# Kernel tuning notes

Measured on AMD Instinct MI355X. Metric: run time of the kernel, lower is better.

Reference implementation:

```python
import jax, jax.numpy as jnp
import numpy as np

N = 8192
IN_C = 128
OUT_C = 128


def setup_inputs() -> dict:
    key = jax.random.key(0)
    k_x, k_adj, k_w, k_b = jax.random.split(key, 4)
    x = jax.random.normal(k_x, (N, IN_C), dtype=jnp.float32)
    adj = jax.random.uniform(k_adj, (N, N), dtype=jnp.float32)
    # nn.Linear params: weight (out, in), bias (out,)
    bound = 1.0 / np.sqrt(IN_C)
    W = jax.random.uniform(k_w, (OUT_C, IN_C), dtype=jnp.float32, minval=-bound, maxval=bound)
    b = jax.random.uniform(k_b, (OUT_C,), dtype=jnp.float32, minval=-bound, maxval=bound)
    return {"x": x, "adj": adj, "W": W, "b": b}


def reference(x, adj, W, b):
    # A_hat = adj + I  (self loops)
    # D_hat = rowsum(A_hat); norm = D^-1/2 A_hat D^-1/2
    n = adj.shape[0]
    a_hat = adj + jnp.eye(n, dtype=adj.dtype)
    deg = jnp.sum(a_hat, axis=1)
    d_inv_sqrt = jnp.power(deg, -0.5)
    d_inv_sqrt = jnp.where(jnp.isinf(d_inv_sqrt), 0.0, d_inv_sqrt)
    # D^-1/2 @ A_hat @ D^-1/2 as row/column broadcast scaling (same math)
    norm_adj = a_hat * d_inv_sqrt[:, None] * d_inv_sqrt[None, :]
    support = norm_adj @ x  # (N, in_c)
    return support @ W.T + b
```

## Files before the change

kernel.cpp:

```cpp
#include <hip/hip_runtime.h>


#define N_ROWS 8192
#define N_C    128
#define NM     (8192 * 128)

typedef __bf16 bf16x8 __attribute__((ext_vector_type(8)));
typedef float  f32x4  __attribute__((ext_vector_type(4)));

__global__ __launch_bounds__(256) void k_rowsum(const float* __restrict__ adj,
                                                float* __restrict__ dinv) {
    const int row = blockIdx.x;
    const float4* rp = (const float4*)(adj + (size_t)row * N_ROWS);
    float s = 0.f;
#pragma unroll
    for (int i = 0; i < 8; ++i) {
        float4 v = rp[threadIdx.x + i * 256];
        s += (v.x + v.y) + (v.z + v.w);
    }
#pragma unroll
    for (int off = 32; off > 0; off >>= 1) s += __shfl_down(s, off, 64);
    __shared__ float red[4];
    const int lane = threadIdx.x & 63, wid = threadIdx.x >> 6;
    if (lane == 0) red[wid] = s;
    __syncthreads();
    if (threadIdx.x == 0) {
        float deg = 1.0f + ((red[0] + red[1]) + (red[2] + red[3]));
        dinv[row] = 1.0f / sqrtf(deg);
    }
}

__global__ __launch_bounds__(256) void k_xw(const float* __restrict__ x,
                                            const float* __restrict__ W,
                                            const float* __restrict__ dinv,
                                            float* __restrict__ tnat,
                                            __bf16* __restrict__ tTh) {
    __shared__ __align__(16) float WtBuf[64 * 132];
    __shared__ __align__(16) float xs[32][128];
    const int tid = threadIdx.x;
    const int j0 = blockIdx.x * 32;

    {
        const int c4 = (tid & 31) * 4;
        const int r0 = tid >> 5;
#pragma unroll
        for (int p = 0; p < 4; ++p)
            *(float4*)&xs[r0 + p * 8][c4] =
                *(const float4*)(x + (size_t)(j0 + r0 + p * 8) * N_C + c4);
    }

    const int tc = tid & 15, tr = tid >> 4;
    const int c0 = tc * 8, r0c = tr * 2;
    float acc[2][8];
#pragma unroll
    for (int i = 0; i < 2; ++i)
#pragma unroll
        for (int j = 0; j < 8; ++j) acc[i][j] = 0.f;

    const int c_lo = (tid & 7) + ((tid >> 7) << 3);
    const int k4   = ((tid >> 3) & 15) * 4;

    for (int kh = 0; kh < 2; ++kh) {
        if (kh) __syncthreads();
#pragma unroll
        for (int p = 0; p < 8; ++p) {
            int c = c_lo + 16 * p;
            float4 w = *(const float4*)(W + (size_t)c * N_C + kh * 64 + k4);
            WtBuf[(k4 + 0) * 132 + c] = w.x;
            WtBuf[(k4 + 1) * 132 + c] = w.y;
            WtBuf[(k4 + 2) * 132 + c] = w.z;
            WtBuf[(k4 + 3) * 132 + c] = w.w;
        }
        __syncthreads();
#pragma unroll 4
        for (int k = 0; k < 64; ++k) {
            const float a0 = xs[r0c][kh * 64 + k];
            const float a1 = xs[r0c + 1][kh * 64 + k];
            const float* wr = &WtBuf[k * 132 + c0];
            const float4 b0 = *(const float4*)wr;
            const float4 b1 = *(const float4*)(wr + 4);
#pragma unroll
            for (int q = 0; q < 4; ++q) {
                acc[0][q]     = fmaf(a0, ((const float*)&b0)[q], acc[0][q]);
                acc[0][q + 4] = fmaf(a0, ((const float*)&b1)[q], acc[0][q + 4]);
                acc[1][q]     = fmaf(a1, ((const float*)&b0)[q], acc[1][q]);
                acc[1][q + 4] = fmaf(a1, ((const float*)&b1)[q], acc[1][q + 4]);
            }
        }
    }

    __syncthreads();
    float* tt = WtBuf;
#pragma unroll
    for (int ri = 0; ri < 2; ++ri) {
        const int j = j0 + r0c + ri;
        const float d = dinv[j];
        float4 o0 = {d * acc[ri][0], d * acc[ri][1], d * acc[ri][2], d * acc[ri][3]};
        float4 o1 = {d * acc[ri][4], d * acc[ri][5], d * acc[ri][6], d * acc[ri][7]};
        *(float4*)(tnat + (size_t)j * N_C + c0)     = o0;
        *(float4*)(tnat + (size_t)j * N_C + c0 + 4) = o1;
#pragma unroll
        for (int q = 0; q < 4; ++q) {
            tt[(r0c + ri) * 129 + c0 + q]     = ((const float*)&o0)[q];
            tt[(r0c + ri) * 129 + c0 + 4 + q] = ((const float*)&o1)[q];
        }
    }
    __syncthreads();
    {
        const int c  = tid >> 1;
        const int jh = (tid & 1) * 16;
        __bf16 ov[16];
#pragma unroll
        for (int q = 0; q < 16; ++q) ov[q] = (__bf16)tt[(jh + q) * 129 + c];
        __bf16* dst = tTh + (size_t)c * N_ROWS + j0 + jh;
        *(int4*)dst = ((const int4*)ov)[0];
        *(int4*)(dst + 8) = ((const int4*)ov)[1];
    }
}

template <bool FUSE>
__global__ __launch_bounds__(512) void k_spmm(const float* __restrict__ adj,
                                              const __bf16* __restrict__ tTh,
                                              const float* __restrict__ tnat,
                                              const float* __restrict__ dinv,
                                              const float* __restrict__ bias,
                                              float* __restrict__ outp,
                                              int klen) {
    __shared__ __align__(16) __bf16 Ah[128 * 72];
    __shared__ __align__(16) __bf16 Al[128 * 72];
    __shared__ __align__(16) __bf16 Th[128 * 72];
    const int tid   = threadIdx.x;
    const int i0    = blockIdx.x * 128;
    const int kbase = blockIdx.y * klen;
    const int nch   = klen / 64;

    float4 areg[2][2];
    int4   treg[2];

    auto load_chunk = [&](int k0) {
#pragma unroll
        for (int p = 0; p < 2; ++p) {
            const int s = tid + p * 512;
            const int r = s >> 3, kg = s & 7;
            const float* g = adj + (size_t)(i0 + r) * N_ROWS + k0 + kg * 8;
            areg[p][0] = *(const float4*)g;
            areg[p][1] = *(const float4*)(g + 4);
        }
        {
            const int n = tid >> 2, q = tid & 3;
            const int4* g = (const int4*)(tTh + (size_t)n * N_ROWS + k0 + q * 16);
            treg[0] = g[0];
            treg[1] = g[1];
        }
    };
    auto store_chunk = [&]() {
#pragma unroll
        for (int p = 0; p < 2; ++p) {
            const int s = tid + p * 512;
            const int r = s >> 3, kg = s & 7;
            __bf16 h[8], lo[8];
            const float* v = (const float*)&areg[p][0];
#pragma unroll
            for (int j = 0; j < 8; ++j) {
                h[j]  = (__bf16)v[j];
                lo[j] = (__bf16)(v[j] - (float)h[j]);
            }
            *(bf16x8*)&Ah[r * 72 + kg * 8] = *(const bf16x8*)h;
            *(bf16x8*)&Al[r * 72 + kg * 8] = *(const bf16x8*)lo;
        }
        {
            const int n = tid >> 2, q = tid & 3;
            *(int4*)&Th[n * 72 + q * 16]     = treg[0];
            *(int4*)&Th[n * 72 + q * 16 + 8] = treg[1];
        }
    };

    const int wv = tid >> 6, l = tid & 63;
    const int wm = wv >> 1, wn = wv & 1;
    const int lm = l & 15, lq = l >> 4;

    f32x4 acc[2][4] = {};

    load_chunk(kbase);
    store_chunk();
    __syncthreads();
    for (int ch = 0; ch < nch; ++ch) {
        const bool more = (ch + 1 < nch);
        if (more) load_chunk(kbase + (ch + 1) * 64);
#pragma unroll
        for (int ks = 0; ks < 2; ++ks) {
            const int ko = ks * 32 + lq * 8;
            bf16x8 a0h = *(const bf16x8*)&Ah[(wm * 32 + lm) * 72 + ko];
            bf16x8 a1h = *(const bf16x8*)&Ah[(wm * 32 + 16 + lm) * 72 + ko];
            bf16x8 a0l = *(const bf16x8*)&Al[(wm * 32 + lm) * 72 + ko];
            bf16x8 a1l = *(const bf16x8*)&Al[(wm * 32 + 16 + lm) * 72 + ko];
#pragma unroll
            for (int nt = 0; nt < 4; ++nt) {
                bf16x8 b = *(const bf16x8*)&Th[(wn * 64 + nt * 16 + lm) * 72 + ko];
                acc[0][nt] = __builtin_amdgcn_mfma_f32_16x16x32_bf16(a0h, b, acc[0][nt], 0, 0, 0);
                acc[1][nt] = __builtin_amdgcn_mfma_f32_16x16x32_bf16(a1h, b, acc[1][nt], 0, 0, 0);
                acc[0][nt] = __builtin_amdgcn_mfma_f32_16x16x32_bf16(a0l, b, acc[0][nt], 0, 0, 0);
                acc[1][nt] = __builtin_amdgcn_mfma_f32_16x16x32_bf16(a1l, b, acc[1][nt], 0, 0, 0);
            }
        }
        __syncthreads();
        if (more) {
            store_chunk();
            __syncthreads();
        }
    }

    float* po = FUSE ? outp : outp + (size_t)blockIdx.y * NM;
#pragma unroll
    for (int mt = 0; mt < 2; ++mt)
#pragma unroll
        for (int nt = 0; nt < 4; ++nt) {
            const int col = wn * 64 + nt * 16 + lm;
#pragma unroll
            for (int r = 0; r < 4; ++r) {
                const int row = i0 + wm * 32 + mt * 16 + lq * 4 + r;
                float v = acc[mt][nt][r];
                if (FUSE)
                    v = dinv[row] * (v + tnat[(size_t)row * N_C + col]) + bias[col];
                po[(size_t)row * N_C + col] = v;
            }
        }
}

__global__ __launch_bounds__(256) void k_combine(const float* __restrict__ part,
                                                 const float* __restrict__ tnat,
                                                 const float* __restrict__ dinv,
                                                 const float* __restrict__ bias,
                                                 float* __restrict__ outp, int S) {
    const size_t off = ((size_t)blockIdx.x * 256 + threadIdx.x) * 4;
    const int i = (int)(off >> 7);
    const int c = (int)(off & 127);
    float4 s = *(const float4*)(tnat + off);
    for (int p = 0; p < S; ++p) {
        const float4 v = *(const float4*)(part + (size_t)p * NM + off);
        s.x += v.x; s.y += v.y; s.z += v.z; s.w += v.w;
    }
    const float d = dinv[i];
    const float4 bv = *(const float4*)(bias + c);
    float4 o = {d * s.x + bv.x, d * s.y + bv.y, d * s.z + bv.z, d * s.w + bv.w};
    *(float4*)(outp + off) = o;
}

extern "C" void kernel_launch(void* const* d_in, const int* in_sizes, int n_in,
                              void* d_out, int out_size, void* d_ws, size_t ws_size,
                              hipStream_t stream) {
    const float* x   = (const float*)d_in[0];
    const float* adj = (const float*)d_in[1];
    const float* W   = (const float*)d_in[2];
    const float* b   = (const float*)d_in[3];
    float* out = (float*)d_out;

    char* base = (char*)d_ws;
    float*  dinv = (float*)base;
    float*  tnat = (float*)(base + 32768);
    __bf16* tTh  = (__bf16*)(base + 32768 + (4u << 20));
    float*  part = (float*)(base + 32768 + (6u << 20));

    const size_t fixed = 32768 + (6u << 20);
    int S = 0;
    if      (ws_size >= fixed + 8 * ((size_t)NM * 4)) S = 8;
    else if (ws_size >= fixed + 4 * ((size_t)NM * 4)) S = 4;
    else if (ws_size >= fixed + 2 * ((size_t)NM * 4)) S = 2;

    k_rowsum<<<N_ROWS, 256, 0, stream>>>(adj, dinv);
    k_xw<<<N_ROWS / 32, 256, 0, stream>>>(x, W, dinv, tnat, tTh);
    if (S > 0) {
        dim3 grid(N_ROWS / 128, S);
        k_spmm<false><<<grid, 512, 0, stream>>>(adj, tTh, tnat, dinv, b, part, N_ROWS / S);
        k_combine<<<NM / 1024, 256, 0, stream>>>(part, tnat, dinv, b, out, S);
    } else {
        dim3 grid(N_ROWS / 128, 1);
        k_spmm<true><<<grid, 512, 0, stream>>>(adj, tTh, tnat, dinv, b, out, N_ROWS);
    }
}
```

Before: 460.1 us.

## Drop split-bf16 adjacency low part and shrink spmm tile to 64 rows

The adjacency matrix was converted to a high/low pair of bf16 values to emulate fp32 accuracy, which doubled the MFMA count and the LDS traffic. It is now converted to a single bf16, which halves the matrix-core work and removes the low-part buffer. The block tile also shrinks from 128 to 64 rows with 256 threads and a 4-block occupancy hint, doubling the grid. The cost is lower precision: uniform adjacency values are rounded to bf16, which may push the result past the tolerance. The smaller tile also means the tTh operand is reloaded by twice as many blocks.

Result: slower. 505.1 us (+9.8%).

```diff
diff --git a/kernel.cpp b/kernel.cpp
--- a/kernel.cpp
+++ b/kernel.cpp
@@ -6,6 +6,7 @@
 #define NM     (8192 * 128)
 
 typedef __bf16 bf16x8 __attribute__((ext_vector_type(8)));
+typedef __bf16 bf16x4 __attribute__((ext_vector_type(4)));
 typedef float  f32x4  __attribute__((ext_vector_type(4)));
 
 __global__ __launch_bounds__(256) void k_rowsum(const float* __restrict__ adj,
@@ -119,60 +120,46 @@
 }
 
 template <bool FUSE>
-__global__ __launch_bounds__(512) void k_spmm(const float* __restrict__ adj,
-                                              const __bf16* __restrict__ tTh,
-                                              const float* __restrict__ tnat,
-                                              const float* __restrict__ dinv,
-                                              const float* __restrict__ bias,
-                                              float* __restrict__ outp,
-                                              int klen) {
-    __shared__ __align__(16) __bf16 Ah[128 * 72];
-    __shared__ __align__(16) __bf16 Al[128 * 72];
+__global__ __launch_bounds__(256, 4) void k_spmm(const float* __restrict__ adj,
+                                                 const __bf16* __restrict__ tTh,
+                                                 const float* __restrict__ tnat,
+                                                 const float* __restrict__ dinv,
+                                                 const float* __restrict__ bias,
+                                                 float* __restrict__ outp,
+                                                 int klen) {
+    __shared__ __align__(16) __bf16 Ah[64 * 72];
     __shared__ __align__(16) __bf16 Th[128 * 72];
     const int tid   = threadIdx.x;
-    const int i0    = blockIdx.x * 128;
+    const int i0    = blockIdx.x * 64;
     const int kbase = blockIdx.y * klen;
     const int nch   = klen / 64;
 
-    float4 areg[2][2];
-    int4   treg[2];
+    float4 areg[4];
+    int4   treg[4];
+
+    const int a_r  = tid >> 4;
+    const int a_ks = (tid & 15) * 4;
+    const int t_n  = tid >> 1;
+    const int t_q  = (tid & 1) * 32;
 
     auto load_chunk = [&](int k0) {
 #pragma unroll
-        for (int p = 0; p < 2; ++p) {
-            const int s = tid + p * 512;
-            const int r = s >> 3, kg = s & 7;
-            const float* g = adj + (size_t)(i0 + r) * N_ROWS + k0 + kg * 8;
-            areg[p][0] = *(const float4*)g;
-            areg[p][1] = *(const float4*)(g + 4);
-        }
-        {
-            const int n = tid >> 2, q = tid & 3;
-            const int4* g = (const int4*)(tTh + (size_t)n * N_ROWS + k0 + q * 16);
-            treg[0] = g[0];
-            treg[1] = g[1];
-        }
+        for (int p = 0; p < 4; ++p)
+            areg[p] = *(const float4*)(adj + (size_t)(i0 + a_r + p * 16) * N_ROWS + k0 + a_ks);
+        const int4* g = (const int4*)(tTh + (size_t)t_n * N_ROWS + k0 + t_q);
+#pragma unroll
+        for (int q = 0; q < 4; ++q) treg[q] = g[q];
     };
     auto store_chunk = [&]() {
 #pragma unroll
-        for (int p = 0; p < 2; ++p) {
-            const int s = tid + p * 512;
-            const int r = s >> 3, kg = s & 7;
-            __bf16 h[8], lo[8];
-            const float* v = (const float*)&areg[p][0];
-#pragma unroll
-            for (int j = 0; j < 8; ++j) {
-                h[j]  = (__bf16)v[j];
-                lo[j] = (__bf16)(v[j] - (float)h[j]);
-            }
-            *(bf16x8*)&Ah[r * 72 + kg * 8] = *(const bf16x8*)h;
-            *(bf16x8*)&Al[r * 72 + kg * 8] = *(const bf16x8*)lo;
-        }
-        {
-            const int n = tid >> 2, q = tid & 3;
-            *(int4*)&Th[n * 72 + q * 16]     = treg[0];
-            *(int4*)&Th[n * 72 + q * 16 + 8] = treg[1];
-        }
+        for (int p = 0; p < 4; ++p) {
+            bf16x4 h = {(__bf16)areg[p].x, (__bf16)areg[p].y,
+                        (__bf16)areg[p].z, (__bf16)areg[p].w};
+            *(bf16x4*)&Ah[(a_r + p * 16) * 72 + a_ks] = h;
+        }
+#pragma unroll
+        for (int q = 0; q < 4; ++q)
+            *(int4*)&Th[t_n * 72 + t_q + q * 8] = treg[q];
     };
 
     const int wv = tid >> 6, l = tid & 63;
@@ -190,17 +177,13 @@
 #pragma unroll
         for (int ks = 0; ks < 2; ++ks) {
             const int ko = ks * 32 + lq * 8;
-            bf16x8 a0h = *(const bf16x8*)&Ah[(wm * 32 + lm) * 72 + ko];
-            bf16x8 a1h = *(const bf16x8*)&Ah[(wm * 32 + 16 + lm) * 72 + ko];
-            bf16x8 a0l = *(const bf16x8*)&Al[(wm * 32 + lm) * 72 + ko];
-            bf16x8 a1l = *(const bf16x8*)&Al[(wm * 32 + 16 + lm) * 72 + ko];
+            bf16x8 a0 = *(const bf16x8*)&Ah[(wm * 32 + lm) * 72 + ko];
+            bf16x8 a1 = *(const bf16x8*)&Ah[(wm * 32 + 16 + lm) * 72 + ko];
 #pragma unroll
             for (int nt = 0; nt < 4; ++nt) {
                 bf16x8 b = *(const bf16x8*)&Th[(wn * 64 + nt * 16 + lm) * 72 + ko];
-                acc[0][nt] = __builtin_amdgcn_mfma_f32_16x16x32_bf16(a0h, b, acc[0][nt], 0, 0, 0);
-                acc[1][nt] = __builtin_amdgcn_mfma_f32_16x16x32_bf16(a1h, b, acc[1][nt], 0, 0, 0);
-                acc[0][nt] = __builtin_amdgcn_mfma_f32_16x16x32_bf16(a0l, b, acc[0][nt], 0, 0, 0);
-                acc[1][nt] = __builtin_amdgcn_mfma_f32_16x16x32_bf16(a1l, b, acc[1][nt], 0, 0, 0);
+                acc[0][nt] = __builtin_amdgcn_mfma_f32_16x16x32_bf16(a0, b, acc[0][nt], 0, 0, 0);
+                acc[1][nt] = __builtin_amdgcn_mfma_f32_16x16x32_bf16(a1, b, acc[1][nt], 0, 0, 0);
             }
         }
         __syncthreads();
@@ -270,11 +253,11 @@
     k_rowsum<<<N_ROWS, 256, 0, stream>>>(adj, dinv);
     k_xw<<<N_ROWS / 32, 256, 0, stream>>>(x, W, dinv, tnat, tTh);
     if (S > 0) {
-        dim3 grid(N_ROWS / 128, S);
-        k_spmm<false><<<grid, 512, 0, stream>>>(adj, tTh, tnat, dinv, b, part, N_ROWS / S);
+        dim3 grid(N_ROWS / 64, S);
+        k_spmm<false><<<grid, 256, 0, stream>>>(adj, tTh, tnat, dinv, b, part, N_ROWS / S);
         k_combine<<<NM / 1024, 256, 0, stream>>>(part, tnat, dinv, b, out, S);
     } else {
-        dim3 grid(N_ROWS / 128, 1);
-        k_spmm<true><<<grid, 512, 0, stream>>>(adj, tTh, tnat, dinv, b, out, N_ROWS);
-    }
-}
+        dim3 grid(N_ROWS / 64, 1);
+        k_spmm<true><<<grid, 256, 0, stream>>>(adj, tTh, tnat, dinv, b, out, N_ROWS);
+    }
+}
```
